# Performance work log

Measured on AMD Instinct MI355X. Metric: run time of the kernel, lower is better.

## Reference

```python
import math
import jax, jax.numpy as jnp
import numpy as np

B, H, T, NH, D = 2, 4, 2048, 8192, 256
THETA = 65536.0  # rope_theta = 2**16
TWO_PI = 2.0 * math.pi


def get_freqs(n, theta):
    # quantize(arange(n), q=2) = floor(i/2)*2, so dim pairs share a frequency
    idx = jnp.arange(n, dtype=jnp.float32)
    q = jnp.floor(idx / 2.0) * 2.0
    return 1.0 / (theta ** (q / n)) / TWO_PI


def rope(phases, v):
    ph = (phases % 1.0) * TWO_PI
    c = jnp.cos(ph)
    s = jnp.sin(ph)
    # interleaved pair rotation: (-v1, v0, -v3, v2, ...)
    v_rot = jnp.stack((-v[..., 1::2], v[..., ::2]), axis=-1).reshape(v.shape)
    return v * c + v_rot * s


def setup_inputs() -> dict:
    key = jax.random.key(0)
    k1, k2, k3 = jax.random.split(key, 3)
    Q = jax.random.normal(k1, (B, H, T, NH), dtype=jnp.float32)
    K = jax.random.normal(k2, (B, H, T, NH), dtype=jnp.float32)
    V = jax.random.normal(k3, (B, 1, T, D), dtype=jnp.float32)
    return {"Q": Q, "K": K, "V": V}


def reference(Q, K, V):
    freqs = get_freqs(NH, THETA).reshape(1, 1, 1, NH)          # [1,1,1,NH]
    t = jnp.arange(T, dtype=jnp.float32).reshape(1, 1, T, 1)    # [1,1,T,1]
    phases = t * freqs                                          # [1,1,T,NH]
    Qr = rope(phases, Q)
    Kr = rope(phases, K)
    scores = jnp.einsum('bhtn,bhsn->bhts', Qr, Kr)              # [B,H,T,T]
    mask = jnp.tril(jnp.ones((T, T), dtype=bool), k=-1)         # strictly lower
    scores = jnp.where(mask, scores, jnp.float32(0.0))
    # V: [B,1,T,D] broadcasts over heads
    return jnp.matmul(scores, V)                                # [B,H,T,D]
```

## Files before the change

kernel.cpp:

```cpp
#include <hip/hip_runtime.h>
#include <hip/hip_bf16.h>

#define B_ 2
#define H_ 4
#define T_ 2048
#define NH_ 8192
#define D_ 256

typedef __attribute__((ext_vector_type(4))) float f32x4;
typedef __attribute__((ext_vector_type(8))) short bf16x8;
typedef __attribute__((ext_vector_type(4))) int i32x4;

__device__ __forceinline__ unsigned short f2bf(float f) {
    union { float f; unsigned u; } v;
    v.f = f;
    unsigned u = v.u;
    unsigned r = u + 0x7FFFu + ((u >> 16) & 1u);
    return (unsigned short)(r >> 16);
}

__global__ __launch_bounds__(256) void rope_cast_kernel(
    const float* __restrict__ Q, const float* __restrict__ K,
    unsigned short* __restrict__ Qb, unsigned short* __restrict__ Kb,
    int bh0)
{
    const long gid = (long)blockIdx.x * 256 + threadIdx.x;
    const int ng = NH_ / 8;
    const int n8 = (int)(gid % ng) * 8;
    const long row = gid / ng;
    const int t = (int)(row % T_);
    const int lbh = (int)(row / T_);

    const long in_off  = ((long)(bh0 + lbh) * T_ + t) * NH_ + n8;
    const long out_off = ((long)lbh * T_ + t) * NH_ + n8;

    float4 qa = *(const float4*)(Q + in_off);
    float4 qb4 = *(const float4*)(Q + in_off + 4);
    float4 ka = *(const float4*)(K + in_off);
    float4 kb4 = *(const float4*)(K + in_off + 4);
    float qv[8] = {qa.x, qa.y, qa.z, qa.w, qb4.x, qb4.y, qb4.z, qb4.w};
    float kv[8] = {ka.x, ka.y, ka.z, ka.w, kb4.x, kb4.y, kb4.z, kb4.w};

    union { i32x4 v; unsigned short u[8]; } qo, ko;
    const int p0 = n8 >> 1;
    const float tf = (float)t;
#pragma unroll
    for (int j = 0; j < 4; ++j) {
        float freq = exp2f(-(float)(p0 + j) * (1.0f / 256.0f)) * 0.15915494309189535f;
        float phase = tf * freq;
        float r = phase - floorf(phase);
        float ph = r * 6.283185307179586f;
        float c = __cosf(ph);
        float s = __sinf(ph);
        float qe = qv[2 * j], qodd = qv[2 * j + 1];
        float ke = kv[2 * j], kodd = kv[2 * j + 1];
        qo.u[2 * j]     = f2bf(qe * c - qodd * s);
        qo.u[2 * j + 1] = f2bf(qodd * c + qe * s);
        ko.u[2 * j]     = f2bf(ke * c - kodd * s);
        ko.u[2 * j + 1] = f2bf(kodd * c + ke * s);
    }
    *(i32x4*)(Qb + out_off) = qo.v;
    *(i32x4*)(Kb + out_off) = ko.v;
}

__global__ __launch_bounds__(256) void vcast_kernel(
    const float* __restrict__ V, unsigned short* __restrict__ Vt)
{
    __shared__ unsigned short tile[64][72];
    const int t0 = blockIdx.x * 64;
    const int d0 = blockIdx.y * 64;
    const int b = blockIdx.z;
    const int tid = threadIdx.x;
#pragma unroll
    for (int rr = 0; rr < 16; ++rr) {
        int tl = rr * 4 + (tid >> 6);
        int dl = tid & 63;
        float v = V[((long)b * T_ + (t0 + tl)) * D_ + d0 + dl];
        tile[dl][tl] = f2bf(v);
    }
    __syncthreads();
#pragma unroll
    for (int rr = 0; rr < 16; ++rr) {
        int dl = rr * 4 + (tid >> 6);
        int tl = tid & 63;
        Vt[((long)b * D_ + (d0 + dl)) * T_ + t0 + tl] = tile[dl][tl];
    }
}

#define GLD16(g, l) __builtin_amdgcn_global_load_lds(                         \
    (const __attribute__((address_space(1))) void*)(g),                       \
    (__attribute__((address_space(3))) void*)(l), 16, 0, 0)

__global__ __launch_bounds__(512, 2) void gemm1_kernel(
    const unsigned short* __restrict__ Qb, const unsigned short* __restrict__ Kb,
    unsigned short* __restrict__ S, float* __restrict__ part, int nFull)
{
    __shared__ __align__(16) unsigned short As[3][256][32];
    __shared__ __align__(16) unsigned short Bs[3][256][32];

    const int wg = blockIdx.x;
    int tileIdx, KT, kc;
    bool full;
    if (wg < nFull) {
        const int xcd = wg & 7, q8 = nFull >> 3, r8 = nFull & 7;
        tileIdx = (xcd < r8 ? xcd * (q8 + 1) : r8 * (q8 + 1) + (xcd - r8) * q8)
                + (wg >> 3);
        KT = 256; kc = 0; full = true;
    } else {
        const int j = wg - nFull;
        tileIdx = nFull + (j >> 3);
        kc = j & 7;
        KT = 32; full = false;
    }
    const int lbh = tileIdx / 36;
    const int t36 = tileIdx % 36;
    int it = (int)((sqrtf(8.0f * (float)t36 + 1.0f) - 1.0f) * 0.5f);
    if ((it + 1) * (it + 2) / 2 <= t36) ++it;
    if (it * (it + 1) / 2 > t36) --it;
    const int jt = t36 - it * (it + 1) / 2;

    const int tid = threadIdx.x;
    const int lane = tid & 63;
    const int wid = tid >> 6;
    const int wr = wid >> 2;
    const int wc = wid & 3;
    const int rofs = lane & 15;
    const int sl8 = (((lane >> 4) ^ ((lane >> 1) & 3))) << 3;

    const int ss8 = (((tid & 3) ^ ((tid >> 3) & 3))) << 3;
    const int dst = tid * 8;
    const long K0 = (long)kc * 1024;
    const unsigned short* Ab = Qb + (long)lbh * T_ * NH_ + (long)it * 256 * NH_ + K0;
    const unsigned short* Bb = Kb + (long)lbh * T_ * NH_ + (long)jt * 256 * NH_ + K0;
    const unsigned short* gA0 = Ab + (long)(tid >> 2) * NH_ + ss8;
    const unsigned short* gA1 = gA0 + 128L * NH_;
    const unsigned short* gB0 = Bb + (long)(tid >> 2) * NH_ + ss8;
    const unsigned short* gB1 = gB0 + 128L * NH_;
    unsigned short* AsB = &As[0][0][0];
    unsigned short* BsB = &Bs[0][0][0];

    f32x4 acc[8][4];
#pragma unroll
    for (int m = 0; m < 8; ++m)
#pragma unroll
        for (int n = 0; n < 4; ++n)
            acc[m][n] = (f32x4){0.f, 0.f, 0.f, 0.f};

#define G256_STAGE(SB, kt) {                                                  \
    const long ko_ = (long)(kt) * 32;                                         \
    GLD16(gA0 + ko_, AsB + (SB) * 8192 + dst);                                \
    GLD16(gA1 + ko_, AsB + (SB) * 8192 + 4096 + dst);                         \
    GLD16(gB0 + ko_, BsB + (SB) * 8192 + dst);                                \
    GLD16(gB1 + ko_, BsB + (SB) * 8192 + 4096 + dst); }

    G256_STAGE(0, 0)
    G256_STAGE(1, 1)
    asm volatile("s_waitcnt vmcnt(4)" ::: "memory");
    __builtin_amdgcn_s_barrier();
    __builtin_amdgcn_sched_barrier(0);

    const int arow = wr * 128 + rofs;
    const int brow = wc * 64 + rofs;
#pragma unroll 1
    for (int t = 0; t < KT; ++t) {
        const int rb = t % 3;
        bf16x8 af[8], bv[4];
        const unsigned short* ab = AsB + rb * 8192 + sl8;
        const unsigned short* bb = BsB + rb * 8192 + sl8;
#pragma unroll
        for (int n = 0; n < 4; ++n)
            bv[n] = *(const bf16x8*)(bb + (brow + n * 16) * 32);
#pragma unroll
        for (int m = 0; m < 8; ++m)
            af[m] = *(const bf16x8*)(ab + (arow + m * 16) * 32);
        if (t + 2 < KT) { const int sb = (t + 2) % 3; G256_STAGE(sb, t + 2) }
        __builtin_amdgcn_s_setprio(1);
#pragma unroll
        for (int m = 0; m < 8; ++m)
#pragma unroll
            for (int n = 0; n < 4; ++n)
                acc[m][n] = __builtin_amdgcn_mfma_f32_16x16x32_bf16(
                    af[m], bv[n], acc[m][n], 0, 0, 0);
        __builtin_amdgcn_s_setprio(0);
        if (t < KT - 2) {
            asm volatile("s_waitcnt vmcnt(4)" ::: "memory");
            __builtin_amdgcn_s_barrier();
            __builtin_amdgcn_sched_barrier(0);
        } else if (t == KT - 2) {
            asm volatile("s_waitcnt vmcnt(0)" ::: "memory");
            __builtin_amdgcn_s_barrier();
            __builtin_amdgcn_sched_barrier(0);
        }
    }

    if (full) {
        unsigned short* Sp = S + (long)lbh * T_ * T_;
        const int r0 = it * 256 + wr * 128 + ((lane >> 4) << 2);
        const int c0 = jt * 256 + wc * 64 + (lane & 15);
#pragma unroll
        for (int m = 0; m < 8; ++m) {
#pragma unroll
            for (int i = 0; i < 4; ++i) {
                const int rr = r0 + m * 16 + i;
#pragma unroll
                for (int n = 0; n < 4; ++n) {
                    const int cc = c0 + n * 16;
                    float v = (cc < rr) ? acc[m][n][i] : 0.0f;
                    Sp[(long)rr * T_ + cc] = f2bf(v);
                }
            }
        }
    } else {
        const int q = tileIdx - nFull;
        float* Pp = part + ((long)(q * 8 + kc)) * 65536;
        const int r0 = wr * 128 + ((lane >> 4) << 2);
        const int c0 = wc * 64 + (lane & 15);
#pragma unroll
        for (int m = 0; m < 8; ++m) {
#pragma unroll
            for (int i = 0; i < 4; ++i) {
                const int rr = r0 + m * 16 + i;
#pragma unroll
                for (int n = 0; n < 4; ++n)
                    Pp[rr * 256 + c0 + n * 16] = acc[m][n][i];
            }
        }
    }
#undef G256_STAGE
}

__global__ __launch_bounds__(256) void reduce_kernel(
    const float* __restrict__ part, unsigned short* __restrict__ S, int nFull)
{
    const int b = blockIdx.x;
    const int q = b >> 6;
    const int e0 = (b & 63) * 1024 + threadIdx.x * 4;
    const int tileIdx = nFull + q;
    const int lbh = tileIdx / 36;
    const int t36 = tileIdx % 36;
    int it = (int)((sqrtf(8.0f * (float)t36 + 1.0f) - 1.0f) * 0.5f);
    if ((it + 1) * (it + 2) / 2 <= t36) ++it;
    if (it * (it + 1) / 2 > t36) --it;
    const int jt = t36 - it * (it + 1) / 2;

    float4 s = {0.f, 0.f, 0.f, 0.f};
#pragma unroll
    for (int kc = 0; kc < 8; ++kc) {
        float4 p = *(const float4*)(part + ((long)(q * 8 + kc)) * 65536 + e0);
        s.x += p.x; s.y += p.y; s.z += p.z; s.w += p.w;
    }
    const int row = e0 >> 8;
    const int col = e0 & 255;
    const int rr = it * 256 + row;
    const int c0 = jt * 256 + col;
    unsigned short o[4];
#pragma unroll
    for (int k = 0; k < 4; ++k) {
        float v = ((c0 + k) < rr) ? ((const float*)&s)[k] : 0.0f;
        o[k] = f2bf(v);
    }
    *(i32x4*)0;
    unsigned short* Sp = S + (long)lbh * T_ * T_ + (long)rr * T_ + c0;
    Sp[0] = o[0]; Sp[1] = o[1]; Sp[2] = o[2]; Sp[3] = o[3];
}

__device__ __forceinline__ void stage_tile(const unsigned short* g, long ldk,
                                           unsigned short* l, int tid)
{
    const int row = tid >> 2;
    const int col = (tid & 3) << 3;
    const unsigned short* g0 = g + (long)row * ldk + col;
    const unsigned short* g1 = g0 + 64 * ldk;
    unsigned short* l0 = l + tid * 8;
    unsigned short* l1 = l0 + 2048;
    GLD16(g0, l0);
    GLD16(g1, l1);
}

__global__ __launch_bounds__(256) void gemm2_kernel(
    const unsigned short* __restrict__ S, const unsigned short* __restrict__ Vt,
    float* __restrict__ Out, int bh0)
{
    const int jn = blockIdx.x;
    const int it = blockIdx.y;
    const int lbh = blockIdx.z;
    const int bh = bh0 + lbh;
    const int b = bh / H_;

    __shared__ __align__(16) unsigned short As2[2][128][32];
    __shared__ __align__(16) unsigned short Bs2[2][128][32];

    const unsigned short* A  = S + (long)lbh * T_ * T_ + (long)it * 128 * T_;
    const unsigned short* Bm = Vt + (long)b * D_ * T_ + (long)jn * 128 * T_;
    const int KT = (it + 1) * 4;

    const int tid = threadIdx.x;
    const int lane = tid & 63;
    const int wid = tid >> 6;
    const int wr = wid >> 1;
    const int wc = wid & 1;
    f32x4 acc[4][4];
#pragma unroll
    for (int m = 0; m < 4; ++m)
#pragma unroll
        for (int n = 0; n < 4; ++n)
            acc[m][n] = (f32x4){0.f, 0.f, 0.f, 0.f};
    const int rofs = lane & 15;
    const int kofs = (lane >> 4) * 8;
    stage_tile(A, T_, &As2[0][0][0], tid);
    stage_tile(Bm, T_, &Bs2[0][0][0], tid);
    int cur = 0;
    for (int kt = 0; kt < KT; ++kt) {
        __syncthreads();
        if (kt + 1 < KT) {
            stage_tile(A + (long)(kt + 1) * 32, T_, &As2[cur ^ 1][0][0], tid);
            stage_tile(Bm + (long)(kt + 1) * 32, T_, &Bs2[cur ^ 1][0][0], tid);
        }
        bf16x8 af[4], bfr[4];
#pragma unroll
        for (int m = 0; m < 4; ++m)
            af[m] = *(const bf16x8*)&As2[cur][wr * 64 + m * 16 + rofs][kofs];
#pragma unroll
        for (int n = 0; n < 4; ++n)
            bfr[n] = *(const bf16x8*)&Bs2[cur][wc * 64 + n * 16 + rofs][kofs];
#pragma unroll
        for (int m = 0; m < 4; ++m)
#pragma unroll
            for (int n = 0; n < 4; ++n)
                acc[m][n] = __builtin_amdgcn_mfma_f32_16x16x32_bf16(
                    af[m], bfr[n], acc[m][n], 0, 0, 0);
        cur ^= 1;
    }

    float* Op = Out + ((long)bh * T_ + it * 128) * D_ + jn * 128;
#pragma unroll
    for (int m = 0; m < 4; ++m) {
        const int rbase = wr * 64 + m * 16 + ((lane >> 4) << 2);
#pragma unroll
        for (int i = 0; i < 4; ++i) {
            const int rr = rbase + i;
#pragma unroll
            for (int n = 0; n < 4; ++n) {
                const int cc = wc * 64 + n * 16 + (lane & 15);
                Op[(long)rr * D_ + cc] = acc[m][n][i];
            }
        }
    }
}

extern "C" void kernel_launch(void* const* d_in, const int* in_sizes, int n_in,
                              void* d_out, int out_size, void* d_ws, size_t ws_size,
                              hipStream_t stream)
{
    const float* Q = (const float*)d_in[0];
    const float* K = (const float*)d_in[1];
    const float* V = (const float*)d_in[2];
    float* Out = (float*)d_out;

    const size_t vt_elems = (size_t)B_ * D_ * T_;
    const size_t part_bytes = 256ull * 65536ull * 4ull;
    auto need = [&](int c, bool split) {
        return 2 * vt_elems + (size_t)c * T_ * NH_ * 2 * 2
             + (size_t)c * T_ * T_ * 2
             + (split ? part_bytes : 0);
    };
    int c; bool split;
    if      (ws_size >= need(8, true))  { c = 8; split = true; }
    else if (ws_size >= need(8, false)) { c = 8; split = false; }
    else if (ws_size >= need(4, false)) { c = 4; split = false; }
    else if (ws_size >= need(2, false)) { c = 2; split = false; }
    else if (ws_size >= need(1, false)) { c = 1; split = false; }
    else return;

    unsigned short* Vt = (unsigned short*)d_ws;
    unsigned short* Qb = Vt + vt_elems;
    unsigned short* Kb = Qb + (size_t)c * T_ * NH_;
    unsigned short* Sb = Kb + (size_t)c * T_ * NH_;
    float* part = (float*)(Sb + (size_t)c * T_ * T_);

    vcast_kernel<<<dim3(T_ / 64, D_ / 64, B_), 256, 0, stream>>>(V, Vt);

    for (int bh0 = 0; bh0 < B_ * H_; bh0 += c) {
        const long groups = (long)c * T_ * (NH_ / 8);
        rope_cast_kernel<<<(int)(groups / 256), 256, 0, stream>>>(Q, K, Qb, Kb, bh0);
        const int nt = 36 * c;
        if (split) {
            const int nFull = nt - 32;
            gemm1_kernel<<<dim3(nFull + 256), 512, 0, stream>>>(Qb, Kb, Sb, part, nFull);
            reduce_kernel<<<dim3(32 * 64), 256, 0, stream>>>(part, Sb, nFull);
        } else {
            gemm1_kernel<<<dim3(nt), 512, 0, stream>>>(Qb, Kb, Sb, part, nt);
        }
        gemm2_kernel<<<dim3(2, 16, c), 256, 0, stream>>>(Sb, Vt, Out, bh0);
    }
}
```

Before: 672.1 us.

## Split last diagonal row of tiles across all heads and use native sin/cos

The split-K scheme now applies to the last four tiles of every head (it=7 row) instead of the last 32 tiles overall. Full tiles are ordered head-interleaved (lbh = bidx&7), and the reduce kernel derives tile coordinates directly. The rope kernel now calls v_sin_f32/v_cos_f32 on the fractional phase, which take their input in revolutions, so the multiply by 2π is dropped. The aim is better load balance across the triangular tile set and cheaper trig. The new split layout hardcodes c=8 and the bottom row of tiles, and the old XCD-aware tile remap is gone.

New measurement: 667.8 us. Within noise of the previous version (-0.6%).

```diff
diff --git a/kernel.cpp b/kernel.cpp
--- a/kernel.cpp
+++ b/kernel.cpp
@@ -49,9 +49,9 @@
         float freq = exp2f(-(float)(p0 + j) * (1.0f / 256.0f)) * 0.15915494309189535f;
         float phase = tf * freq;
         float r = phase - floorf(phase);
-        float ph = r * 6.283185307179586f;
-        float c = __cosf(ph);
-        float s = __sinf(ph);
+        float c, s;
+        asm("v_cos_f32 %0, %1" : "=v"(c) : "v"(r));
+        asm("v_sin_f32 %0, %1" : "=v"(s) : "v"(r));
         float qe = qv[2 * j], qodd = qv[2 * j + 1];
         float ke = kv[2 * j], kodd = kv[2 * j + 1];
         qo.u[2 * j]     = f2bf(qe * c - qodd * s);
@@ -93,27 +93,28 @@
 
 __global__ __launch_bounds__(512, 2) void gemm1_kernel(
     const unsigned short* __restrict__ Qb, const unsigned short* __restrict__ Kb,
-    unsigned short* __restrict__ S, float* __restrict__ part, int nFull)
+    unsigned short* __restrict__ S, float* __restrict__ part, int split)
 {
     __shared__ __align__(16) unsigned short As[3][256][32];
     __shared__ __align__(16) unsigned short Bs[3][256][32];
 
-    const int wg = blockIdx.x;
-    int tileIdx, KT, kc;
+    const int bidx = blockIdx.x;
+    int lbh, t36, KT, kc, pidx;
     bool full;
-    if (wg < nFull) {
-        const int xcd = wg & 7, q8 = nFull >> 3, r8 = nFull & 7;
-        tileIdx = (xcd < r8 ? xcd * (q8 + 1) : r8 * (q8 + 1) + (xcd - r8) * q8)
-                + (wg >> 3);
-        KT = 256; kc = 0; full = true;
+    if (split) {
+        lbh = bidx & 7;
+        const int s = bidx >> 3;
+        if (s < 32) { t36 = s; KT = 256; kc = 0; full = true; pidx = 0; }
+        else {
+            const int j = s - 32;
+            t36 = 32 + (j >> 3);
+            kc = j & 7;
+            KT = 32; full = false;
+            pidx = (lbh * 4 + (t36 - 32)) * 8 + kc;
+        }
     } else {
-        const int j = wg - nFull;
-        tileIdx = nFull + (j >> 3);
-        kc = j & 7;
-        KT = 32; full = false;
-    }
-    const int lbh = tileIdx / 36;
-    const int t36 = tileIdx % 36;
+        lbh = bidx / 36; t36 = bidx % 36; KT = 256; kc = 0; full = true; pidx = 0;
+    }
     int it = (int)((sqrtf(8.0f * (float)t36 + 1.0f) - 1.0f) * 0.5f);
     if ((it + 1) * (it + 2) / 2 <= t36) ++it;
     if (it * (it + 1) / 2 > t36) --it;
@@ -211,8 +212,7 @@
             }
         }
     } else {
-        const int q = tileIdx - nFull;
-        float* Pp = part + ((long)(q * 8 + kc)) * 65536;
+        float* Pp = part + (long)pidx * 65536;
         const int r0 = wr * 128 + ((lane >> 4) << 2);
         const int c0 = wc * 64 + (lane & 15);
 #pragma unroll
@@ -230,18 +230,14 @@
 }
 
 __global__ __launch_bounds__(256) void reduce_kernel(
-    const float* __restrict__ part, unsigned short* __restrict__ S, int nFull)
+    const float* __restrict__ part, unsigned short* __restrict__ S)
 {
     const int b = blockIdx.x;
     const int q = b >> 6;
     const int e0 = (b & 63) * 1024 + threadIdx.x * 4;
-    const int tileIdx = nFull + q;
-    const int lbh = tileIdx / 36;
-    const int t36 = tileIdx % 36;
-    int it = (int)((sqrtf(8.0f * (float)t36 + 1.0f) - 1.0f) * 0.5f);
-    if ((it + 1) * (it + 2) / 2 <= t36) ++it;
-    if (it * (it + 1) / 2 > t36) --it;
-    const int jt = t36 - it * (it + 1) / 2;
+    const int lbh = q >> 2;
+    const int jt = 4 + (q & 3);
+    const int it = 7;
 
     float4 s = {0.f, 0.f, 0.f, 0.f};
 #pragma unroll
@@ -259,7 +255,6 @@
         float v = ((c0 + k) < rr) ? ((const float*)&s)[k] : 0.0f;
         o[k] = f2bf(v);
     }
-    *(i32x4*)0;
     unsigned short* Sp = S + (long)lbh * T_ * T_ + (long)rr * T_ + c0;
     Sp[0] = o[0]; Sp[1] = o[1]; Sp[2] = o[2]; Sp[3] = o[3];
 }
@@ -383,13 +378,11 @@
     for (int bh0 = 0; bh0 < B_ * H_; bh0 += c) {
         const long groups = (long)c * T_ * (NH_ / 8);
         rope_cast_kernel<<<(int)(groups / 256), 256, 0, stream>>>(Q, K, Qb, Kb, bh0);
-        const int nt = 36 * c;
         if (split) {
-            const int nFull = nt - 32;
-            gemm1_kernel<<<dim3(nFull + 256), 512, 0, stream>>>(Qb, Kb, Sb, part, nFull);
-            reduce_kernel<<<dim3(32 * 64), 256, 0, stream>>>(part, Sb, nFull);
+            gemm1_kernel<<<dim3(512), 512, 0, stream>>>(Qb, Kb, Sb, part, 1);
+            reduce_kernel<<<dim3(32 * 64), 256, 0, stream>>>(part, Sb);
         } else {
-            gemm1_kernel<<<dim3(nt), 512, 0, stream>>>(Qb, Kb, Sb, part, nt);
+            gemm1_kernel<<<dim3(36 * c), 512, 0, stream>>>(Qb, Kb, Sb, part, 0);
         }
         gemm2_kernel<<<dim3(2, 16, c), 256, 0, stream>>>(Sb, Vt, Out, bh0);
     }
```
